# Performance work log

Measured on AMD Instinct MI355X. Metric: run time of the kernel, lower is better.

Reference implementation:

```python
import jax, jax.numpy as jnp
import numpy as np

N = 50000          # nodes
E = 1250000        # edges (no self loops in raw data)
H = 2              # heads
C = 32             # out channels per head
DIN = 64           # dim_node
ED = 16            # edge_dim
G = 16             # graphs in batch
NC = 5             # num classes
SLOPE = 0.2        # GATConv leaky_relu negative_slope


def _glorot(key, shape):
    fan = shape[0] if len(shape) == 2 else shape[-1]
    return jax.random.normal(key, shape, jnp.float32) * (1.0 / np.sqrt(fan))


def setup_inputs() -> dict:
    key = jax.random.key(0)
    ks = jax.random.split(key, 24)
    x = jax.random.normal(ks[0], (N, DIN), jnp.float32)
    dst = jax.random.randint(ks[1], (E,), 0, N)
    off = jax.random.randint(ks[2], (E,), 1, N)
    src = (dst + off) % N  # guarantees src != dst (PyG removes self loops before re-adding)
    edge_index = jnp.stack([src, dst]).astype(jnp.int32)
    edge_attr = jax.random.normal(ks[3], (E, ED), jnp.float32)
    batch = jnp.sort(jax.random.randint(ks[4], (N,), 0, G)).astype(jnp.int32)
    inp = dict(x=x, edge_index=edge_index, edge_attr=edge_attr, batch=batch)
    # layer 1: in=DIN, heads=H, out=C, concat -> H*C
    inp["W1"] = _glorot(ks[5], (DIN, H * C)); inp["asrc1"] = _glorot(ks[6], (H, C))
    inp["adst1"] = _glorot(ks[7], (H, C)); inp["We1"] = _glorot(ks[8], (ED, H * C))
    inp["ae1"] = _glorot(ks[9], (H, C)); inp["b1"] = jnp.zeros((H * C,), jnp.float32)
    # layer 2: in=H*C, heads=H, out=C, concat
    inp["W2"] = _glorot(ks[10], (H * C, H * C)); inp["asrc2"] = _glorot(ks[11], (H, C))
    inp["adst2"] = _glorot(ks[12], (H, C)); inp["We2"] = _glorot(ks[13], (ED, H * C))
    inp["ae2"] = _glorot(ks[14], (H, C)); inp["b2"] = jnp.zeros((H * C,), jnp.float32)
    # layer 3: in=H*C, heads=1, out=C, concat=False
    inp["W3"] = _glorot(ks[15], (H * C, C)); inp["asrc3"] = _glorot(ks[16], (1, C))
    inp["adst3"] = _glorot(ks[17], (1, C)); inp["We3"] = _glorot(ks[18], (ED, C))
    inp["ae3"] = _glorot(ks[19], (1, C)); inp["b3"] = jnp.zeros((C,), jnp.float32)
    # ffn: Linear(C, NC) + softmax (dropout is identity in eval)
    inp["Wf"] = _glorot(ks[20], (C, NC)); inp["bf"] = jnp.zeros((NC,), jnp.float32)
    return inp


def _gat_layer(h_in, src, dst, eattr, W, asrc, adst, We, ae, b, heads, out, concat):
    n = h_in.shape[0]
    h = (h_in @ W).reshape(n, heads, out)                      # [N,H,C]
    s_src = jnp.einsum('nhc,hc->nh', h, asrc)                  # per-node src scores
    s_dst = jnp.einsum('nhc,hc->nh', h, adst)
    he = (eattr @ We).reshape(-1, heads, out)                  # [E,H,C]
    s_e = jnp.einsum('ehc,hc->eh', he, ae)
    logit = jax.nn.leaky_relu(s_src[src] + s_dst[dst] + s_e, SLOPE)  # [E,H]
    m = jax.ops.segment_max(logit, dst, num_segments=n)
    ex = jnp.exp(logit - m[dst])
    den = jax.ops.segment_sum(ex, dst, num_segments=n)
    alpha = ex / (den[dst] + 1e-16)                            # segment softmax per dst node
    agg = jax.ops.segment_sum(h[src] * alpha[..., None], dst, num_segments=n)  # [N,H,C]
    out_x = agg.reshape(n, heads * out) if concat else agg.mean(axis=1)
    return out_x + b


def _gat_forward(x, edge_index, edge_attr, batch,
                 W1, asrc1, adst1, We1, ae1, b1,
                 W2, asrc2, adst2, We2, ae2, b2,
                 W3, asrc3, adst3, We3, ae3, b3,
                 Wf, bf):
    src, dst = edge_index[0], edge_index[1]
    n = x.shape[0]
    # add_self_loops with fill_value='mean': self-loop edge_attr = mean of incoming edge_attr
    deg = jax.ops.segment_sum(jnp.ones((src.shape[0],), x.dtype), dst, num_segments=n)
    self_attr = jax.ops.segment_sum(edge_attr, dst, num_segments=n) / jnp.maximum(deg, 1.0)[:, None]
    loop = jnp.arange(n, dtype=src.dtype)
    src_a = jnp.concatenate([src, loop])
    dst_a = jnp.concatenate([dst, loop])
    eattr_a = jnp.concatenate([edge_attr, self_attr], axis=0)

    h = jax.nn.relu(_gat_layer(x, src_a, dst_a, eattr_a, W1, asrc1, adst1, We1, ae1, b1, H, C, True))
    h = jax.nn.relu(_gat_layer(h, src_a, dst_a, eattr_a, W2, asrc2, adst2, We2, ae2, b2, H, C, True))
    h = jax.nn.relu(_gat_layer(h, src_a, dst_a, eattr_a, W3, asrc3, adst3, We3, ae3, b3, 1, C, False))

    # global mean pool per graph
    cnt = jax.ops.segment_sum(jnp.ones((n,), h.dtype), batch, num_segments=G)
    pooled = jax.ops.segment_sum(h, batch, num_segments=G) / jnp.maximum(cnt, 1.0)[:, None]
    # ffn: Dropout (identity at eval) -> Linear -> Softmax(dim=1)
    return jax.nn.softmax(pooled @ Wf + bf, axis=1)


def reference(x, edge_index, edge_attr, batch,
              W1, asrc1, adst1, We1, ae1, b1,
              W2, asrc2, adst2, We2, ae2, b2,
              W3, asrc3, adst3, We3, ae3, b3,
              Wf, bf):
    return _gat_forward(x, edge_index, edge_attr, batch,
                        W1, asrc1, adst1, We1, ae1, b1,
                        W2, asrc2, adst2, We2, ae2, b2,
                        W3, asrc3, adst3, We3, ae3, b3,
                        Wf, bf)
```

## Files before the change

kernel.cpp:

```cpp
#include <hip/hip_runtime.h>
#include <math.h>

#define NN 50000
#define EE 1250000
#define GG 16
#define NCLS 5
#define NBIN 391
#define BINSHIFT 7
#define CAPB 3900

constexpr size_t AL(size_t x){ return (x + 255) & ~size_t(255); }
constexpr size_t OFF_ROWPTR = 0;
constexpr size_t OFF_CURS   = OFF_ROWPTR + AL((size_t)(NN+1)*4);
constexpr size_t OFF_SRCS   = OFF_CURS + AL(4096);
constexpr size_t OFF_SE12   = OFF_SRCS + AL((size_t)EE*2);
constexpr size_t OFF_SE34   = OFF_SE12 + AL((size_t)EE*4);
constexpr size_t OFF_SE5    = OFF_SE34 + AL((size_t)EE*4);
constexpr size_t OFF_SSRC   = OFF_SE5 + AL((size_t)EE*2);
constexpr size_t OFF_SDST   = OFF_SSRC + AL((size_t)NN*2*4);
constexpr size_t OFF_STAG   = OFF_SDST + AL((size_t)NN*2*4);
constexpr size_t OFF_BUFH   = OFF_STAG + AL((size_t)NBIN*CAPB*16);
constexpr size_t OFF_BUFO   = OFF_BUFH + AL((size_t)NN*32*4);
constexpr size_t OFF_WEFF   = OFF_BUFO + AL((size_t)NN*64*4);
constexpr size_t OFF_POOL   = OFF_WEFF + AL(80*4);

__device__ __forceinline__ float leaky(float x){ return x > 0.f ? x : 0.2f*x; }
__device__ __forceinline__ unsigned rne_bf16(float x){
    unsigned u = __float_as_uint(x);
    return (u + 0x7FFFu + ((u >> 16) & 1u)) >> 16;
}
__device__ __forceinline__ float bf16lo(unsigned p){ return __uint_as_float(p << 16); }
__device__ __forceinline__ float bf16hi(unsigned p){ return __uint_as_float(p & 0xFFFF0000u); }

__global__ void weffbinit_kernel(const float* __restrict__ We1, const float* __restrict__ ae1,
                                 const float* __restrict__ We2, const float* __restrict__ ae2,
                                 const float* __restrict__ We3, const float* __restrict__ ae3,
                                 float* __restrict__ weff, int* __restrict__ bincursor){
    int t = threadIdx.x;
    if (t < NBIN) bincursor[t] = t*CAPB;
    if (t >= 80) return;
    int j = t >> 4, d = t & 15;
    const float* We; const float* ae; int hc, h;
    if (j == 0){ We = We1; ae = ae1; hc = 64; h = 0; }
    else if (j == 1){ We = We1; ae = ae1; hc = 64; h = 1; }
    else if (j == 2){ We = We2; ae = ae2; hc = 64; h = 0; }
    else if (j == 3){ We = We2; ae = ae2; hc = 64; h = 1; }
    else { We = We3; ae = ae3; hc = 32; h = 0; }
    float s = 0.f;
    for (int c = 0; c < 32; ++c) s += We[d*hc + h*32 + c] * ae[h*32 + c];
    weff[j*16 + d] = s;
}

__global__ void binA_kernel(const int* __restrict__ src, const int* __restrict__ dst,
                            const float* __restrict__ eattr, const float* __restrict__ weff,
                            int* __restrict__ bincursor, int4* __restrict__ staging, int nE){
    __shared__ int lcount[NBIN];
    __shared__ int lbase[NBIN];
    __shared__ float w[80];
    int tid = threadIdx.x;
    if (tid < 80) w[tid] = weff[tid];
    for (int i = tid; i < NBIN; i += 1024) lcount[i] = 0;
    __syncthreads();
    int base = blockIdx.x * 4096;
    int w0[4], bn[4], idx[4]; unsigned p01[4], p23[4], p4[4];
    #pragma unroll
    for (int k = 0; k < 4; ++k){
        int i = base + k*1024 + tid;
        if (i < nE){
            int d = dst[i];
            int s = src[i];
            bn[k]  = d >> BINSHIFT;
            w0[k]  = s | ((d & 127) << 16);
            const float4* row = (const float4*)(eattr + (size_t)i*16);
            float4 a0 = row[0], a1 = row[1], a2 = row[2], a3 = row[3];
            float a[16] = {a0.x,a0.y,a0.z,a0.w, a1.x,a1.y,a1.z,a1.w,
                           a2.x,a2.y,a2.z,a2.w, a3.x,a3.y,a3.z,a3.w};
            float sj[5];
            #pragma unroll
            for (int j = 0; j < 5; ++j){
                float s2 = 0.f;
                #pragma unroll
                for (int d2 = 0; d2 < 16; ++d2) s2 += a[d2]*w[j*16+d2];
                sj[j] = s2;
            }
            p01[k] = rne_bf16(sj[0]) | (rne_bf16(sj[1]) << 16);
            p23[k] = rne_bf16(sj[2]) | (rne_bf16(sj[3]) << 16);
            p4[k]  = rne_bf16(sj[4]);
            idx[k] = atomicAdd(&lcount[bn[k]], 1);
        } else bn[k] = -1;
    }
    __syncthreads();
    for (int i = tid; i < NBIN; i += 1024){
        int c = lcount[i];
        lbase[i] = c ? atomicAdd(&bincursor[i], c) : 0;
    }
    __syncthreads();
    #pragma unroll
    for (int k = 0; k < 4; ++k)
        if (bn[k] >= 0)
            staging[lbase[bn[k]] + idx[k]] = make_int4(w0[k], (int)p01[k], (int)p23[k], (int)p4[k]);
}

__global__ void binscan_kernel(const int* __restrict__ bincursor, int* __restrict__ binbase){
    __shared__ int s[512];
    int tid = threadIdx.x;
    int v = (tid < NBIN) ? (bincursor[tid] - tid*CAPB) : 0;
    s[tid] = v;
    __syncthreads();
    for (int off = 1; off < 512; off <<= 1){
        int t = (tid >= off) ? s[tid-off] : 0;
        __syncthreads();
        s[tid] += t;
        __syncthreads();
    }
    if (tid < NBIN) binbase[tid] = s[tid] - v;
}

__global__ void binB_kernel(const int* __restrict__ bincursor, const int* __restrict__ binbase,
                            const int4* __restrict__ staging,
                            unsigned short* __restrict__ srcs, unsigned* __restrict__ se12,
                            unsigned* __restrict__ se34, unsigned short* __restrict__ se5,
                            int* __restrict__ rowptr, int nN){
    __shared__ int4 lout[CAPB];
    __shared__ int lcnt[128];
    __shared__ int lpre[128];
    int b = blockIdx.x;
    int sbase = b*CAPB;
    int cnt = bincursor[b] - sbase;
    int tid = threadIdx.x;
    if (tid < 128) lcnt[tid] = 0;
    __syncthreads();
    for (int k = tid; k < cnt; k += 1024)
        atomicAdd(&lcnt[staging[sbase + k].x >> 16], 1);
    __syncthreads();
    if (tid < 64){
        int a0 = lcnt[2*tid], a1 = lcnt[2*tid+1];
        int pair = a0 + a1, incl = pair;
        #pragma unroll
        for (int off = 1; off < 64; off <<= 1){
            int t = __shfl_up(incl, off);
            if (tid >= off) incl += t;
        }
        int base0 = incl - pair;
        lpre[2*tid] = base0;
        lpre[2*tid+1] = base0 + a0;
    }
    __syncthreads();
    int r0 = binbase[b];
    int lo = b << BINSHIFT;
    if (tid < 128 && lo + tid < nN) rowptr[lo + tid] = r0 + lpre[tid];
    if (b == NBIN-1 && tid == 0) rowptr[nN] = r0 + cnt;
    if (tid < 128) lcnt[tid] = 0;
    __syncthreads();
    for (int k = tid; k < cnt; k += 1024){
        int4 v = staging[sbase + k];
        int dl = v.x >> 16;
        int rank = atomicAdd(&lcnt[dl], 1);
        v.x &= 0xFFFF;
        lout[lpre[dl] + rank] = v;
    }
    __syncthreads();
    for (int k = tid; k < cnt; k += 1024){
        int4 v = lout[k];
        srcs[r0 + k] = (unsigned short)v.x;
        se12[r0 + k] = (unsigned)v.y;
        se34[r0 + k] = (unsigned)v.z;
        se5[r0 + k]  = (unsigned short)v.w;
    }
}

template<int OUTC>
__global__ void transform_kernel(const float* __restrict__ in, const float* __restrict__ W,
                                 const float* __restrict__ asrc, const float* __restrict__ adst,
                                 unsigned* __restrict__ hout2, float* __restrict__ ssrc,
                                 float* __restrict__ sdst, int nN){
    constexpr int R = 256/OUTC;
    __shared__ float Ws[64*OUTC];
    __shared__ float ins[R*64];
    int tid = threadIdx.x;
    for (int i = tid; i < 64*OUTC; i += 256) Ws[i] = W[i];
    int base = blockIdx.x * R;
    for (int i = tid; i < R*64; i += 256){
        int n = base + i/64;
        ins[i] = (n < nN) ? in[(size_t)n*64 + (i & 63)] : 0.f;
    }
    __syncthreads();
    int r = tid / OUTC, c = tid % OUTC;
    int n = base + r;
    float acc = 0.f;
    #pragma unroll
    for (int d = 0; d < 64; ++d) acc += ins[r*64 + d] * Ws[d*OUTC + c];
    float ps = acc * asrc[c];
    float pd = acc * adst[c];
    #pragma unroll
    for (int m = 1; m <= 16; m <<= 1){ ps += __shfl_xor(ps, m); pd += __shfl_xor(pd, m); }
    float accN = __shfl_xor(acc, 1);
    if (n < nN){
        if ((c & 1) == 0){
            unsigned pk = rne_bf16(acc) | (rne_bf16(accN) << 16);
            hout2[(size_t)n*(OUTC/2) + (c >> 1)] = pk;
        }
        constexpr int HEADS = OUTC/32;
        if ((c & 31) == 0){
            int h = c >> 5;
            ssrc[n*HEADS + h] = ps;
            sdst[n*HEADS + h] = pd;
        }
    }
}

template<int OUTC>
__global__ void agg_kernel(const int* __restrict__ rowptr, const unsigned short* __restrict__ srcs,
                           const unsigned* __restrict__ sePa, const unsigned short* __restrict__ sePb,
                           const float* __restrict__ ssrc, const float* __restrict__ sdst,
                           const unsigned* __restrict__ hbuf2, const float* __restrict__ bias,
                           float* __restrict__ outbuf, int nN){
    constexpr int HEADS = OUTC/32;
    constexpr int HALF  = OUTC/4;
    constexpr int EPI   = 64/HALF;
    int wid = threadIdx.x >> 6;
    int lane = threadIdx.x & 63;
    int n = blockIdx.x*4 + wid;
    if (n >= nN) return;
    int row_start = rowptr[n], row_end = rowptr[n+1];
    int degn = row_end - row_start;
    float sd0 = sdst[n*HEADS + 0];
    float sd1 = (HEADS == 2) ? sdst[n*HEADS + 1] : 0.f;

    int sub = lane / HALF;
    int lc  = lane & (HALF - 1);
    int h   = (HEADS == 2) ? ((4*lc) >> 5) : 0;

    float acc0=0.f, acc1=0.f, acc2=0.f, acc3=0.f, den=0.f;
    float ssp0=0.f, ssp1=0.f;
    const uint2* hb2 = (const uint2*)hbuf2;

    for (int p0 = row_start; p0 < row_end; p0 += 64){
        int myp = p0 + lane;
        int srcreg = 0; unsigned wpk = 0; float w0s = 0.f;
        if (myp < row_end){
            srcreg = srcs[myp];
            if (HEADS == 2){
                unsigned pk = sePa[myp];
                float e0 = bf16lo(pk);
                float e1 = bf16hi(pk);
                ssp0 += e0; ssp1 += e1;
                float2 sv = ((const float2*)ssrc)[srcreg];
                float w0 = __expf(leaky(sv.x + sd0 + e0));
                float w1 = __expf(leaky(sv.y + sd1 + e1));
                wpk = rne_bf16(w0) | (rne_bf16(w1) << 16);
            } else {
                float e0 = __uint_as_float(((unsigned)sePb[myp]) << 16);
                ssp0 += e0;
                w0s = __expf(leaky(ssrc[srcreg] + sd0 + e0));
            }
        }
        int cnt = min(64, row_end - p0);
        #pragma unroll 2
        for (int q = sub; q < cnt; q += EPI){
            int sj = __shfl(srcreg, q);
            float wj;
            if (HEADS == 2){
                unsigned wq = __shfl(wpk, q);
                wj = h ? bf16hi(wq) : bf16lo(wq);
            } else {
                wj = __shfl(w0s, q);
            }
            den += wj;
            uint2 hv = hb2[(size_t)sj*(OUTC/4) + lc];
            acc0 += wj * bf16lo(hv.x);
            acc1 += wj * bf16hi(hv.x);
            acc2 += wj * bf16lo(hv.y);
            acc3 += wj * bf16hi(hv.y);
        }
    }

    #pragma unroll
    for (int m = HALF; m < 64; m <<= 1){
        acc0 += __shfl_xor(acc0, m); acc1 += __shfl_xor(acc1, m);
        acc2 += __shfl_xor(acc2, m); acc3 += __shfl_xor(acc3, m);
        den  += __shfl_xor(den, m);
    }
    #pragma unroll
    for (int m = 1; m < 64; m <<= 1){
        ssp0 += __shfl_xor(ssp0, m);
        if (HEADS == 2) ssp1 += __shfl_xor(ssp1, m);
    }

    float invdeg = 1.f / (float)max(degn, 1);
    float srh = ssrc[n*HEADS + h];
    float sdh = h ? sd1 : sd0;
    float ssh = h ? ssp1 : ssp0;
    float wself = __expf(leaky(srh + sdh + ssh*invdeg));
    uint2 hv = hb2[(size_t)n*(OUTC/4) + lc];
    acc0 += wself * bf16lo(hv.x); acc1 += wself * bf16hi(hv.x);
    acc2 += wself * bf16lo(hv.y); acc3 += wself * bf16hi(hv.y);
    den += wself;

    if (lane < HALF){
        float inv = 1.f / (den + 1e-16f);
        float4 o;
        o.x = fmaxf(acc0*inv + bias[4*lc+0], 0.f);
        o.y = fmaxf(acc1*inv + bias[4*lc+1], 0.f);
        o.z = fmaxf(acc2*inv + bias[4*lc+2], 0.f);
        o.w = fmaxf(acc3*inv + bias[4*lc+3], 0.f);
        ((float4*)outbuf)[(size_t)n*(OUTC/4) + lc] = o;
    }
}

__global__ void pool_kernel(const float* __restrict__ h3, const int* __restrict__ batch,
                            float* __restrict__ pool, float* __restrict__ cnt, int nN){
    __shared__ float accs[GG*32];
    __shared__ float acccnt[GG];
    int tid = threadIdx.x;
    for (int i = tid; i < GG*32; i += 256) accs[i] = 0.f;
    if (tid < GG) acccnt[tid] = 0.f;
    __syncthreads();
    int r = tid >> 5, c = tid & 31;
    int base = blockIdx.x * 512;
    int end = min(base + 512, nN);
    for (int n = base + r; n < end; n += 8){
        int g = batch[n];
        atomicAdd(&accs[g*32 + c], h3[(size_t)n*32 + c]);
        if (c == 0) atomicAdd(&acccnt[g], 1.f);
    }
    __syncthreads();
    for (int i = tid; i < GG*32; i += 256) atomicAdd(&pool[i], accs[i]);
    if (tid < GG) atomicAdd(&cnt[tid], acccnt[tid]);
}

__global__ void final_kernel(const float* __restrict__ pool, const float* __restrict__ cnt,
                             const float* __restrict__ Wf, const float* __restrict__ bf,
                             float* __restrict__ out){
    int g = threadIdx.x;
    if (g >= GG) return;
    float ic = 1.f / fmaxf(cnt[g], 1.f);
    float lg[NCLS];
    #pragma unroll
    for (int k = 0; k < NCLS; ++k) lg[k] = bf[k];
    for (int c = 0; c < 32; ++c){
        float v = pool[g*32 + c] * ic;
        #pragma unroll
        for (int k = 0; k < NCLS; ++k) lg[k] += v * Wf[c*NCLS + k];
    }
    float mx = lg[0];
    #pragma unroll
    for (int k = 1; k < NCLS; ++k) mx = fmaxf(mx, lg[k]);
    float sum = 0.f, ex[NCLS];
    #pragma unroll
    for (int k = 0; k < NCLS; ++k){ ex[k] = expf(lg[k] - mx); sum += ex[k]; }
    #pragma unroll
    for (int k = 0; k < NCLS; ++k) out[g*NCLS + k] = ex[k]/sum;
}

extern "C" void kernel_launch(void* const* d_in, const int* in_sizes, int n_in,
                              void* d_out, int out_size, void* d_ws, size_t ws_size,
                              hipStream_t stream){
    const float* x     = (const float*)d_in[0];
    const int*   eidx  = (const int*)d_in[1];
    const float* eattr = (const float*)d_in[2];
    const int*   batch = (const int*)d_in[3];
    const float* W1 = (const float*)d_in[4];  const float* asrc1 = (const float*)d_in[5];
    const float* adst1 = (const float*)d_in[6]; const float* We1 = (const float*)d_in[7];
    const float* ae1 = (const float*)d_in[8];  const float* b1 = (const float*)d_in[9];
    const float* W2 = (const float*)d_in[10]; const float* asrc2 = (const float*)d_in[11];
    const float* adst2 = (const float*)d_in[12]; const float* We2 = (const float*)d_in[13];
    const float* ae2 = (const float*)d_in[14]; const float* b2 = (const float*)d_in[15];
    const float* W3 = (const float*)d_in[16]; const float* asrc3 = (const float*)d_in[17];
    const float* adst3 = (const float*)d_in[18]; const float* We3 = (const float*)d_in[19];
    const float* ae3 = (const float*)d_in[20]; const float* b3 = (const float*)d_in[21];
    const float* Wf = (const float*)d_in[22]; const float* bf = (const float*)d_in[23];
    float* out = (float*)d_out;

    char* ws = (char*)d_ws;
    int*   rowptr = (int*)(ws + OFF_ROWPTR);
    int*   curs   = (int*)(ws + OFF_CURS);
    unsigned short* srcs = (unsigned short*)(ws + OFF_SRCS);
    unsigned* se12 = (unsigned*)(ws + OFF_SE12);
    unsigned* se34 = (unsigned*)(ws + OFF_SE34);
    unsigned short* se5 = (unsigned short*)(ws + OFF_SE5);
    float* ssrc   = (float*)(ws + OFF_SSRC);
    float* sdst   = (float*)(ws + OFF_SDST);
    int4*  staging = (int4*)(ws + OFF_STAG);
    unsigned* bufH = (unsigned*)(ws + OFF_BUFH);
    float* bufO   = (float*)(ws + OFF_BUFO);
    float* weff   = (float*)(ws + OFF_WEFF);
    float* pool   = (float*)(ws + OFF_POOL);
    float* cnt    = pool + GG*32;

    int* bincursor = curs;
    int* binbase   = curs + 512;

    const int* srcA = eidx;
    const int* dstA = eidx + EE;

    hipMemsetAsync(pool, 0, (GG*32 + GG)*4, stream);

    weffbinit_kernel<<<1, 512, 0, stream>>>(We1, ae1, We2, ae2, We3, ae3, weff, bincursor);
    binA_kernel<<<(EE + 4095)/4096, 1024, 0, stream>>>(srcA, dstA, eattr, weff, bincursor, staging, EE);
    binscan_kernel<<<1, 512, 0, stream>>>(bincursor, binbase);
    binB_kernel<<<NBIN, 1024, 0, stream>>>(bincursor, binbase, staging, srcs, se12, se34, se5, rowptr, NN);

    int ngrid4 = (NN + 3)/4;
    int ngrid8 = (NN + 7)/8;
    transform_kernel<64><<<ngrid4, 256, 0, stream>>>(x, W1, asrc1, adst1, bufH, ssrc, sdst, NN);
    agg_kernel<64><<<ngrid4, 256, 0, stream>>>(rowptr, srcs, se12, nullptr,
                                               ssrc, sdst, bufH, b1, bufO, NN);
    transform_kernel<64><<<ngrid4, 256, 0, stream>>>(bufO, W2, asrc2, adst2, bufH, ssrc, sdst, NN);
    agg_kernel<64><<<ngrid4, 256, 0, stream>>>(rowptr, srcs, se34, nullptr,
                                               ssrc, sdst, bufH, b2, bufO, NN);
    transform_kernel<32><<<ngrid8, 256, 0, stream>>>(bufO, W3, asrc3, adst3, bufH, ssrc, sdst, NN);
    agg_kernel<32><<<ngrid4, 256, 0, stream>>>(rowptr, srcs, nullptr, se5,
                                               ssrc, sdst, bufH, b3, bufO, NN);
    pool_kernel<<<(NN + 511)/512, 256, 0, stream>>>(bufO, batch, pool, cnt, NN);
    final_kernel<<<1, 64, 0, stream>>>(pool, cnt, Wf, bf, out);
}
```

Measured before the change: 273.2 us.

## Fold weff and bin-scan kernels into binning kernels to cut launches

Removes the separate weff/bin-init kernel by computing the effective edge-attention weights inside each binA block, and zeroes the bin counters through the existing memset. Removes the bin scan kernel by having each binB block sum the counts of all preceding bins itself. It also halves the number of edges per binA block, doubling the grid. This trades redundant per-block weight computation and prefix summation for two fewer kernel launches and their serialization gaps.

```diff
diff --git a/kernel.cpp b/kernel.cpp
--- a/kernel.cpp
+++ b/kernel.cpp
@@ -11,8 +11,7 @@
 
 constexpr size_t AL(size_t x){ return (x + 255) & ~size_t(255); }
 constexpr size_t OFF_ROWPTR = 0;
-constexpr size_t OFF_CURS   = OFF_ROWPTR + AL((size_t)(NN+1)*4);
-constexpr size_t OFF_SRCS   = OFF_CURS + AL(4096);
+constexpr size_t OFF_SRCS   = OFF_ROWPTR + AL((size_t)(NN+1)*4);
 constexpr size_t OFF_SE12   = OFF_SRCS + AL((size_t)EE*2);
 constexpr size_t OFF_SE34   = OFF_SE12 + AL((size_t)EE*4);
 constexpr size_t OFF_SE5    = OFF_SE34 + AL((size_t)EE*4);
@@ -21,8 +20,7 @@
 constexpr size_t OFF_STAG   = OFF_SDST + AL((size_t)NN*2*4);
 constexpr size_t OFF_BUFH   = OFF_STAG + AL((size_t)NBIN*CAPB*16);
 constexpr size_t OFF_BUFO   = OFF_BUFH + AL((size_t)NN*32*4);
-constexpr size_t OFF_WEFF   = OFF_BUFO + AL((size_t)NN*64*4);
-constexpr size_t OFF_POOL   = OFF_WEFF + AL(80*4);
+constexpr size_t OFF_POOL   = OFF_BUFO + AL((size_t)NN*64*4);
 
 __device__ __forceinline__ float leaky(float x){ return x > 0.f ? x : 0.2f*x; }
 __device__ __forceinline__ unsigned rne_bf16(float x){
@@ -32,39 +30,34 @@
 __device__ __forceinline__ float bf16lo(unsigned p){ return __uint_as_float(p << 16); }
 __device__ __forceinline__ float bf16hi(unsigned p){ return __uint_as_float(p & 0xFFFF0000u); }
 
-__global__ void weffbinit_kernel(const float* __restrict__ We1, const float* __restrict__ ae1,
-                                 const float* __restrict__ We2, const float* __restrict__ ae2,
-                                 const float* __restrict__ We3, const float* __restrict__ ae3,
-                                 float* __restrict__ weff, int* __restrict__ bincursor){
-    int t = threadIdx.x;
-    if (t < NBIN) bincursor[t] = t*CAPB;
-    if (t >= 80) return;
-    int j = t >> 4, d = t & 15;
-    const float* We; const float* ae; int hc, h;
-    if (j == 0){ We = We1; ae = ae1; hc = 64; h = 0; }
-    else if (j == 1){ We = We1; ae = ae1; hc = 64; h = 1; }
-    else if (j == 2){ We = We2; ae = ae2; hc = 64; h = 0; }
-    else if (j == 3){ We = We2; ae = ae2; hc = 64; h = 1; }
-    else { We = We3; ae = ae3; hc = 32; h = 0; }
-    float s = 0.f;
-    for (int c = 0; c < 32; ++c) s += We[d*hc + h*32 + c] * ae[h*32 + c];
-    weff[j*16 + d] = s;
-}
-
 __global__ void binA_kernel(const int* __restrict__ src, const int* __restrict__ dst,
-                            const float* __restrict__ eattr, const float* __restrict__ weff,
+                            const float* __restrict__ eattr,
+                            const float* __restrict__ We1, const float* __restrict__ ae1,
+                            const float* __restrict__ We2, const float* __restrict__ ae2,
+                            const float* __restrict__ We3, const float* __restrict__ ae3,
                             int* __restrict__ bincursor, int4* __restrict__ staging, int nE){
     __shared__ int lcount[NBIN];
     __shared__ int lbase[NBIN];
     __shared__ float w[80];
     int tid = threadIdx.x;
-    if (tid < 80) w[tid] = weff[tid];
+    if (tid < 80){
+        int j = tid >> 4, d = tid & 15;
+        const float* We; const float* ae; int hc, h;
+        if (j == 0){ We = We1; ae = ae1; hc = 64; h = 0; }
+        else if (j == 1){ We = We1; ae = ae1; hc = 64; h = 1; }
+        else if (j == 2){ We = We2; ae = ae2; hc = 64; h = 0; }
+        else if (j == 3){ We = We2; ae = ae2; hc = 64; h = 1; }
+        else { We = We3; ae = ae3; hc = 32; h = 0; }
+        float s = 0.f;
+        for (int c = 0; c < 32; ++c) s += We[d*hc + h*32 + c] * ae[h*32 + c];
+        w[tid] = s;
+    }
     for (int i = tid; i < NBIN; i += 1024) lcount[i] = 0;
     __syncthreads();
-    int base = blockIdx.x * 4096;
-    int w0[4], bn[4], idx[4]; unsigned p01[4], p23[4], p4[4];
-    #pragma unroll
-    for (int k = 0; k < 4; ++k){
+    int base = blockIdx.x * 2048;
+    int w0[2], bn[2], idx[2]; unsigned p01[2], p23[2], p4[2];
+    #pragma unroll
+    for (int k = 0; k < 2; ++k){
         int i = base + k*1024 + tid;
         if (i < nE){
             int d = dst[i];
@@ -92,43 +85,35 @@
     __syncthreads();
     for (int i = tid; i < NBIN; i += 1024){
         int c = lcount[i];
-        lbase[i] = c ? atomicAdd(&bincursor[i], c) : 0;
-    }
-    __syncthreads();
-    #pragma unroll
-    for (int k = 0; k < 4; ++k)
+        lbase[i] = c ? (i*CAPB + atomicAdd(&bincursor[i], c)) : 0;
+    }
+    __syncthreads();
+    #pragma unroll
+    for (int k = 0; k < 2; ++k)
         if (bn[k] >= 0)
             staging[lbase[bn[k]] + idx[k]] = make_int4(w0[k], (int)p01[k], (int)p23[k], (int)p4[k]);
 }
 
-__global__ void binscan_kernel(const int* __restrict__ bincursor, int* __restrict__ binbase){
-    __shared__ int s[512];
-    int tid = threadIdx.x;
-    int v = (tid < NBIN) ? (bincursor[tid] - tid*CAPB) : 0;
-    s[tid] = v;
-    __syncthreads();
-    for (int off = 1; off < 512; off <<= 1){
-        int t = (tid >= off) ? s[tid-off] : 0;
-        __syncthreads();
-        s[tid] += t;
-        __syncthreads();
-    }
-    if (tid < NBIN) binbase[tid] = s[tid] - v;
-}
-
-__global__ void binB_kernel(const int* __restrict__ bincursor, const int* __restrict__ binbase,
-                            const int4* __restrict__ staging,
+__global__ void binB_kernel(const int* __restrict__ bincursor, const int4* __restrict__ staging,
                             unsigned short* __restrict__ srcs, unsigned* __restrict__ se12,
                             unsigned* __restrict__ se34, unsigned short* __restrict__ se5,
                             int* __restrict__ rowptr, int nN){
     __shared__ int4 lout[CAPB];
     __shared__ int lcnt[128];
     __shared__ int lpre[128];
+    __shared__ int sbb;
     int b = blockIdx.x;
     int sbase = b*CAPB;
-    int cnt = bincursor[b] - sbase;
+    int cnt = bincursor[b];
     int tid = threadIdx.x;
     if (tid < 128) lcnt[tid] = 0;
+    if (tid < 64){
+        int sum = 0;
+        for (int i = tid; i < b; i += 64) sum += bincursor[i];
+        #pragma unroll
+        for (int m = 1; m < 64; m <<= 1) sum += __shfl_xor(sum, m);
+        if (tid == 0) sbb = sum;
+    }
     __syncthreads();
     for (int k = tid; k < cnt; k += 1024)
         atomicAdd(&lcnt[staging[sbase + k].x >> 16], 1);
@@ -146,10 +131,10 @@
         lpre[2*tid+1] = base0 + a0;
     }
     __syncthreads();
-    int r0 = binbase[b];
+    int r0 = sbb;
     int lo = b << BINSHIFT;
     if (tid < 128 && lo + tid < nN) rowptr[lo + tid] = r0 + lpre[tid];
-    if (b == NBIN-1 && tid == 0) rowptr[nN] = r0 + cnt;
+    if (b == 0 && tid == 0) rowptr[nN] = EE;
     if (tid < 128) lcnt[tid] = 0;
     __syncthreads();
     for (int k = tid; k < cnt; k += 1024){
@@ -374,7 +359,6 @@
 
     char* ws = (char*)d_ws;
     int*   rowptr = (int*)(ws + OFF_ROWPTR);
-    int*   curs   = (int*)(ws + OFF_CURS);
     unsigned short* srcs = (unsigned short*)(ws + OFF_SRCS);
     unsigned* se12 = (unsigned*)(ws + OFF_SE12);
     unsigned* se34 = (unsigned*)(ws + OFF_SE34);
@@ -384,22 +368,19 @@
     int4*  staging = (int4*)(ws + OFF_STAG);
     unsigned* bufH = (unsigned*)(ws + OFF_BUFH);
     float* bufO   = (float*)(ws + OFF_BUFO);
-    float* weff   = (float*)(ws + OFF_WEFF);
     float* pool   = (float*)(ws + OFF_POOL);
     float* cnt    = pool + GG*32;
-
-    int* bincursor = curs;
-    int* binbase   = curs + 512;
+    int*   bincursor = (int*)(cnt + GG);
 
     const int* srcA = eidx;
     const int* dstA = eidx + EE;
 
-    hipMemsetAsync(pool, 0, (GG*32 + GG)*4, stream);
-
-    weffbinit_kernel<<<1, 512, 0, stream>>>(We1, ae1, We2, ae2, We3, ae3, weff, bincursor);
-    binA_kernel<<<(EE + 4095)/4096, 1024, 0, stream>>>(srcA, dstA, eattr, weff, bincursor, staging, EE);
-    binscan_kernel<<<1, 512, 0, stream>>>(bincursor, binbase);
-    binB_kernel<<<NBIN, 1024, 0, stream>>>(bincursor, binbase, staging, srcs, se12, se34, se5, rowptr, NN);
+    hipMemsetAsync(pool, 0, (GG*32 + GG)*4 + NBIN*4, stream);
+
+    binA_kernel<<<(EE + 2047)/2048, 1024, 0, stream>>>(srcA, dstA, eattr,
+                                                       We1, ae1, We2, ae2, We3, ae3,
+                                                       bincursor, staging, EE);
+    binB_kernel<<<NBIN, 1024, 0, stream>>>(bincursor, staging, srcs, se12, se34, se5, rowptr, NN);
 
     int ngrid4 = (NN + 3)/4;
     int ngrid8 = (NN + 7)/8;
```

Result: faster. 266.0 us (-2.6%).
